# Optimization experiments

Measured on AMD Instinct MI355X. Metric: run time of the kernel, lower is better.

## Reference

```python
import jax, jax.numpy as jnp
import numpy as np

WEIGHT = 6.0  # fixed self.weight in the module


def setup_inputs() -> dict:
    key = jax.random.key(0)
    k1, k2 = jax.random.split(key)
    B, C = 131072, 1000
    op = jax.random.normal(k1, (B, C), dtype=jnp.float32)
    target = jax.random.randint(k2, (B,), 0, C, dtype=jnp.int64)
    return {"op": op, "target": target}


def reference(op, target):
    # scaled, max-stabilized softmax complement: 1 - softmax(weight * op)
    # then gather the target class per sample and take the mean over batch.
    B = op.shape[0]
    sm = jax.nn.softmax(op * WEIGHT, axis=1)          # [B, C]
    picked = jnp.take_along_axis(sm, target[:, None], axis=1)[:, 0]  # [B]
    loss = jnp.sum(1.0 - picked) / B
    return loss.reshape(1)  # torch returns a shape-[1] tensor
```

## Files before the change

### kernel.cpp

```cpp
#include <hip/hip_runtime.h>
#include <math.h>


#define WEIGHT 6.0f
#define LOG2E  1.4426950408889634f

constexpr int C     = 1000;
constexpr int QUADS = C / 4;

typedef float fx4 __attribute__((ext_vector_type(4)));

__global__ __launch_bounds__(256) void steploss_rows(
    const float* __restrict__ op, const int* __restrict__ tgt,
    float* __restrict__ partials, int B)
{
    const int wave = threadIdx.x >> 6;
    const int lane = threadIdx.x & 63;
    const int row  = blockIdx.x * 4 + wave;

    __shared__ float lds[4];

    const float W2 = WEIGHT * LOG2E;

    fx4 v[4];
    int ti = 0;
    if (row < B) {
        const fx4* rp = reinterpret_cast<const fx4*>(op + (size_t)row * C);
        #pragma unroll
        for (int it = 0; it < 4; ++it) {
            int idx = it * 64 + lane;
            if (idx < QUADS) {
                v[it] = __builtin_nontemporal_load(rp + idx);
            } else {
                v[it] = (fx4){-INFINITY, -INFINITY, -INFINITY, -INFINITY};
            }
        }
        ti = tgt[row];
    } else {
        #pragma unroll
        for (int it = 0; it < 4; ++it)
            v[it] = (fx4){-INFINITY, -INFINITY, -INFINITY, -INFINITY};
    }

    const int  q    = ti >> 2;
    const bool own  = (lane == (q & 63));
    const int  slot = ((q >> 6) << 2) | (ti & 3);

    float s = 0.f, sel = 0.f;
    #pragma unroll
    for (int it = 0; it < 4; ++it) {
        #pragma unroll
        for (int j = 0; j < 4; ++j) {
            const int i = it * 4 + j;
            float e = __builtin_amdgcn_exp2f(v[it][j] * W2);
            s += e;
            if (own && i == slot) sel = e;
        }
    }

    #pragma unroll
    for (int off = 1; off < 64; off <<= 1) {
        s   += __shfl_xor(s,   off, 64);
        sel += __shfl_xor(sel, off, 64);
    }

    if (lane == 0) {
        float part = 0.f;
        if (row < B) part = 1.0f - sel / s;
        lds[wave] = part;
    }
    __syncthreads();
    if (threadIdx.x == 0)
        partials[blockIdx.x] = (lds[0] + lds[1]) + (lds[2] + lds[3]);
}

__global__ __launch_bounds__(1024) void steploss_reduce(
    const float* __restrict__ partials, float* __restrict__ out,
    int n, float inv_b)
{
    __shared__ float lds[1024];
    float s = 0.f;
    for (int i = threadIdx.x; i < n; i += 1024)
        s += partials[i];
    lds[threadIdx.x] = s;
    __syncthreads();
    #pragma unroll
    for (int off = 512; off >= 64; off >>= 1) {
        if (threadIdx.x < off) lds[threadIdx.x] += lds[threadIdx.x + off];
        __syncthreads();
    }
    if (threadIdx.x < 64) {
        float w = lds[threadIdx.x];
        #pragma unroll
        for (int off = 1; off < 64; off <<= 1)
            w += __shfl_xor(w, off, 64);
        if (threadIdx.x == 0) out[0] = w * inv_b;
    }
}

extern "C" void kernel_launch(void* const* d_in, const int* in_sizes, int n_in,
                              void* d_out, int out_size, void* d_ws, size_t ws_size,
                              hipStream_t stream)
{
    const float* op  = (const float*)d_in[0];
    const int*   tgt = (const int*)  d_in[1];
    float*       out = (float*)d_out;

    const int B       = in_sizes[1];
    const int nblocks = (B + 3) / 4;

    float* partials = (float*)d_ws;

    steploss_rows<<<nblocks, 256, 0, stream>>>(op, tgt, partials, B);
    steploss_reduce<<<1, 1024, 0, stream>>>(partials, out, nblocks, 1.0f / (float)B);
}
```

Baseline: 92.81 us.

## Process multiple rows per wave with fixed grid and simplify final reduction

Switches from one wave per row with a block per four rows to a fixed grid of 2048 blocks where each wave loops over several consecutive rows, accumulating sel/s locally. It drops the per-row sel shuffle reduction, uses a fast reciprocal, and moves the 1-minus into the final reduction, which now uses wave shuffles over 256 threads. The aim is to cut block launch and tail overhead and per-row reduction work. The cost is that rows within a wave are processed serially, so load latency is hidden only by occupancy across waves.

```diff
diff --git a/kernel.cpp b/kernel.cpp
--- a/kernel.cpp
+++ b/kernel.cpp
@@ -10,92 +10,88 @@
 
 typedef float fx4 __attribute__((ext_vector_type(4)));
 
-__global__ __launch_bounds__(256) void steploss_rows(
+__global__ __launch_bounds__(256, 8) void steploss_rows(
     const float* __restrict__ op, const int* __restrict__ tgt,
-    float* __restrict__ partials, int B)
+    float* __restrict__ partials, int B, int rpw)
 {
     const int wave = threadIdx.x >> 6;
     const int lane = threadIdx.x & 63;
-    const int row  = blockIdx.x * 4 + wave;
+    __builtin_assume(lane < 64);
+    const int w = blockIdx.x * 4 + wave;
 
     __shared__ float lds[4];
 
     const float W2 = WEIGHT * LOG2E;
 
-    fx4 v[4];
-    int ti = 0;
-    if (row < B) {
+    float acc = 0.f;
+
+    const int row0 = w * rpw;
+    for (int r = 0; r < rpw; ++r) {
+        const int row = row0 + r;
+        if (row >= B) break;
+
         const fx4* rp = reinterpret_cast<const fx4*>(op + (size_t)row * C);
+        fx4 v[4];
         #pragma unroll
         for (int it = 0; it < 4; ++it) {
             int idx = it * 64 + lane;
-            if (idx < QUADS) {
+            if (it < 3 || idx < QUADS) {
                 v[it] = __builtin_nontemporal_load(rp + idx);
             } else {
                 v[it] = (fx4){-INFINITY, -INFINITY, -INFINITY, -INFINITY};
             }
         }
-        ti = tgt[row];
-    } else {
+        const int ti = tgt[row];
+
+        const int  q    = ti >> 2;
+        const bool own  = (lane == (q & 63));
+        const int  slot = ((q >> 6) << 2) | (ti & 3);
+
+        float s = 0.f, sel = 0.f;
         #pragma unroll
-        for (int it = 0; it < 4; ++it)
-            v[it] = (fx4){-INFINITY, -INFINITY, -INFINITY, -INFINITY};
-    }
+        for (int it = 0; it < 4; ++it) {
+            #pragma unroll
+            for (int j = 0; j < 4; ++j) {
+                const int i = it * 4 + j;
+                float e = __builtin_amdgcn_exp2f(v[it][j] * W2);
+                s += e;
+                if (own && i == slot) sel = e;
+            }
+        }
+        #pragma unroll
+        for (int off = 1; off < 64; off <<= 1)
+            s += __shfl_xor(s, off, 64);
 
-    const int  q    = ti >> 2;
-    const bool own  = (lane == (q & 63));
-    const int  slot = ((q >> 6) << 2) | (ti & 3);
-
-    float s = 0.f, sel = 0.f;
-    #pragma unroll
-    for (int it = 0; it < 4; ++it) {
-        #pragma unroll
-        for (int j = 0; j < 4; ++j) {
-            const int i = it * 4 + j;
-            float e = __builtin_amdgcn_exp2f(v[it][j] * W2);
-            s += e;
-            if (own && i == slot) sel = e;
-        }
+        acc += sel * __builtin_amdgcn_rcpf(s);
     }
 
     #pragma unroll
-    for (int off = 1; off < 64; off <<= 1) {
-        s   += __shfl_xor(s,   off, 64);
-        sel += __shfl_xor(sel, off, 64);
-    }
+    for (int off = 1; off < 64; off <<= 1)
+        acc += __shfl_xor(acc, off, 64);
 
-    if (lane == 0) {
-        float part = 0.f;
-        if (row < B) part = 1.0f - sel / s;
-        lds[wave] = part;
-    }
+    if (lane == 0) lds[wave] = acc;
     __syncthreads();
     if (threadIdx.x == 0)
         partials[blockIdx.x] = (lds[0] + lds[1]) + (lds[2] + lds[3]);
 }
 
-__global__ __launch_bounds__(1024) void steploss_reduce(
+__global__ __launch_bounds__(256) void steploss_reduce(
     const float* __restrict__ partials, float* __restrict__ out,
     int n, float inv_b)
 {
-    __shared__ float lds[1024];
     float s = 0.f;
-    for (int i = threadIdx.x; i < n; i += 1024)
+    for (int i = threadIdx.x; i < n; i += 256)
         s += partials[i];
-    lds[threadIdx.x] = s;
+    __shared__ float lds[4];
+    #pragma unroll
+    for (int off = 1; off < 64; off <<= 1)
+        s += __shfl_xor(s, off, 64);
+    const int wave = threadIdx.x >> 6;
+    const int lane = threadIdx.x & 63;
+    if (lane == 0) lds[wave] = s;
     __syncthreads();
-    #pragma unroll
-    for (int off = 512; off >= 64; off >>= 1) {
-        if (threadIdx.x < off) lds[threadIdx.x] += lds[threadIdx.x + off];
-        __syncthreads();
-    }
-    if (threadIdx.x < 64) {
-        float w = lds[threadIdx.x];
-        #pragma unroll
-        for (int off = 1; off < 64; off <<= 1)
-            w += __shfl_xor(w, off, 64);
-        if (threadIdx.x == 0) out[0] = w * inv_b;
-    }
+    if (threadIdx.x == 0)
+        out[0] = 1.0f - ((lds[0] + lds[1]) + (lds[2] + lds[3])) * inv_b;
 }
 
 extern "C" void kernel_launch(void* const* d_in, const int* in_sizes, int n_in,
@@ -107,10 +103,12 @@
     float*       out = (float*)d_out;
 
     const int B       = in_sizes[1];
-    const int nblocks = (B + 3) / 4;
+    const int nblocks = 2048;
+    const int nwaves  = nblocks * 4;
+    const int rpw     = (B + nwaves - 1) / nwaves;
 
     float* partials = (float*)d_ws;
 
-    steploss_rows<<<nblocks, 256, 0, stream>>>(op, tgt, partials, B);
-    steploss_reduce<<<1, 1024, 0, stream>>>(partials, out, nblocks, 1.0f / (float)B);
+    steploss_rows<<<nblocks, 256, 0, stream>>>(op, tgt, partials, B, rpw);
+    steploss_reduce<<<1, 256, 0, stream>>>(partials, out, nblocks, 1.0f / (float)B);
 }
```

After: 86.80 us. 1.07x faster.
